# Optimization experiments

Hardware: AMD Instinct MI355X
Metric: run time of the kernel (lower is better)

The kernel has to match this reference:

```python
import jax, jax.numpy as jnp
import numpy as np

N = 100000   # nodes
E = 1600000  # edges (avg degree 16)
IN, HID, OUT = 128, 128, 64


def _glorot(key, shape):
    limit = np.sqrt(6.0 / (shape[0] + shape[1])).astype(np.float32)
    return jax.random.uniform(key, shape, jnp.float32, -limit, limit)


def setup_inputs() -> dict:
    key = jax.random.key(0)
    ks = jax.random.split(key, 12)
    inp = {}
    for i, (f, s, d) in enumerate([("feat1", "src1", "dst1"), ("feat2", "src2", "dst2"), ("feat", "src", "dst")]):
        inp[f] = jax.random.normal(ks[3 * i], (N, IN), jnp.float32)
        inp[s] = jax.random.randint(ks[3 * i + 1], (E,), 0, N, jnp.int32)
        inp[d] = jax.random.randint(ks[3 * i + 2], (E,), 0, N, jnp.int32)
    inp["W1"] = _glorot(ks[9], (IN, HID))
    inp["b1"] = jnp.zeros((HID,), jnp.float32)
    inp["W2"] = _glorot(ks[10], (HID, OUT))
    inp["b2"] = jnp.zeros((OUT,), jnp.float32)
    return inp


def _gcn_layer(x, src, dst, W, b):
    # DGL GraphConv norm='both': D_dst^{-1/2} * A * D_src^{-1/2} * X * W + b
    ones = jnp.ones(src.shape, jnp.float32)
    deg_out = jax.ops.segment_sum(ones, src, num_segments=N)
    deg_in = jax.ops.segment_sum(ones, dst, num_segments=N)
    norm_src = jax.lax.rsqrt(jnp.maximum(deg_out, 1.0))
    norm_dst = jax.lax.rsqrt(jnp.maximum(deg_in, 1.0))
    h = (x @ W) * norm_src[:, None]           # transform then normalize (math-equivalent order)
    agg = jax.ops.segment_sum(h[src], dst, num_segments=N)  # spmm aggregate
    return agg * norm_dst[:, None] + b


def _encoder(x, src, dst, W1, b1, W2, b2):
    h = jax.nn.relu(_gcn_layer(x, src, dst, W1, b1))
    return _gcn_layer(h, src, dst, W2, b2)


def reference(feat1, src1, dst1, feat2, src2, dst2, feat, src, dst, W1, b1, W2, b2):
    z1 = _encoder(feat1, src1, dst1, W1, b1, W2, b2)
    z2 = _encoder(feat2, src2, dst2, W1, b1, W2, b2)
    z = _encoder(feat, src, dst, W1, b1, W2, b2)
    return (z1, z2, z)
```

## Files before the change

### kernel.cpp

```cpp
#include <hip/hip_runtime.h>

#define NNODES 100000
#define NEDGES 1600000
#define FIN 128
#define FHID 128
#define FOUT 64

typedef unsigned short u16;
typedef unsigned char u8;
typedef unsigned int u32;
typedef __attribute__((ext_vector_type(8))) short short8;
typedef __attribute__((ext_vector_type(4))) float floatx4;

#define NBUK 391
#define NSL2 250
#define SLICE2 (NEDGES / NSL2)
#define SP ((size_t)NSL2 * NBUK)
#define NH16 ((size_t)NNODES * FHID)

__device__ __forceinline__ u16 f2bf(float f) {
  u32 u = __float_as_uint(f);
  u32 r = (u + 0x7fffu + ((u >> 16) & 1u)) >> 16;
  return (u16)r;
}

__device__ __forceinline__ const int* sel(const int* a, const int* b, const int* c, int z) {
  return z == 0 ? a : (z == 1 ? b : c);
}


__global__ __launch_bounds__(256) void bucket_hist_kernel(
    const int* s0, const int* s1, const int* s2,
    const int* d0, const int* d1, const int* d2,
    u16* __restrict__ Hbase, int E) {
  const int z = blockIdx.z;
  const int* __restrict__ src = sel(s0, s1, s2, z);
  const int* __restrict__ dst = sel(d0, d1, d2, z);
  u32* __restrict__ part = (u32*)(Hbase + (size_t)z * NH16);
  u32* __restrict__ part_src = part + SP;
  __shared__ u32 hd[NBUK], hs[NBUK];
  const int s = blockIdx.x;
  for (int i = threadIdx.x; i < NBUK; i += 256) { hd[i] = 0; hs[i] = 0; }
  __syncthreads();
  const int e0 = s * SLICE2, e1 = min(e0 + SLICE2, E);
  const int i0 = e0 >> 2, i1 = e1 >> 2;
  for (int i = i0 + threadIdx.x; i < i1; i += 256) {
    int4 dv = ((const int4*)dst)[i];
    int4 sv = ((const int4*)src)[i];
    atomicAdd(&hd[(u32)dv.x >> 8], 1u);
    atomicAdd(&hd[(u32)dv.y >> 8], 1u);
    atomicAdd(&hd[(u32)dv.z >> 8], 1u);
    atomicAdd(&hd[(u32)dv.w >> 8], 1u);
    atomicAdd(&hs[(u32)sv.x >> 8], 1u);
    atomicAdd(&hs[(u32)sv.y >> 8], 1u);
    atomicAdd(&hs[(u32)sv.z >> 8], 1u);
    atomicAdd(&hs[(u32)sv.w >> 8], 1u);
  }
  __syncthreads();
  for (int i = threadIdx.x; i < NBUK; i += 256) {
    part[(size_t)s * NBUK + i] = hd[i];
    part_src[(size_t)s * NBUK + i] = hs[i];
  }
}

__global__ __launch_bounds__(512) void scan_part_kernel(u16* __restrict__ Hbase,
                                                        u32* __restrict__ boff_d,
                                                        u32* __restrict__ bcount_d,
                                                        u32* __restrict__ boff_s,
                                                        u32* __restrict__ bcount_s) {
  const int z = blockIdx.z;
  u32* base = (u32*)(Hbase + (size_t)z * NH16);
  u32* __restrict__ part = blockIdx.x ? base + SP : base;
  u32* __restrict__ boff = (blockIdx.x ? boff_s : boff_d) + (size_t)z * NBUK;
  u32* __restrict__ bcount = (blockIdx.x ? bcount_s : bcount_d) + (size_t)z * NBUK;
  const int b = threadIdx.x;
  u32 run = 0;
  if (b < NBUK) {
#pragma unroll 5
    for (int s = 0; s < NSL2; s++) {
      u32 v = part[(size_t)s * NBUK + b];
      part[(size_t)s * NBUK + b] = run;
      run += v;
    }
  }
  __shared__ u32 sh[512];
  sh[threadIdx.x] = (b < NBUK) ? run : 0;
  __syncthreads();
  for (int d = 1; d < 512; d <<= 1) {
    u32 t = (threadIdx.x >= d) ? sh[threadIdx.x - d] : 0;
    __syncthreads();
    sh[threadIdx.x] += t;
    __syncthreads();
  }
  if (b < NBUK) {
    boff[b] = sh[threadIdx.x] - run;
    bcount[b] = run;
  }
}

__global__ __launch_bounds__(256) void scatter_kernel(
    const int* s0, const int* s1, const int* s2,
    const int* d0, const int* d1, const int* d2,
    u16* __restrict__ Hbase, u16* __restrict__ Tbase,
    const u32* __restrict__ boff_d, const u32* __restrict__ boff_src, int E) {
  const int z = blockIdx.z;
  const int* __restrict__ src = sel(s0, s1, s2, z);
  const int* __restrict__ dst = sel(d0, d1, d2, z);
  const u32* __restrict__ part = (const u32*)(Hbase + (size_t)z * NH16);
  const u32* __restrict__ part_src = part + SP;
  u8* __restrict__ pes = (u8*)(part_src + SP);
  u32* __restrict__ pe = (u32*)(Tbase + (size_t)z * NH16);
  const u32* __restrict__ boff = boff_d + (size_t)z * NBUK;
  const u32* __restrict__ boff_s = boff_src + (size_t)z * NBUK;
  __shared__ u32 cur[NBUK], curs[NBUK];
  const int s = blockIdx.x;
  for (int i = threadIdx.x; i < NBUK; i += 256) {
    cur[i] = part[(size_t)s * NBUK + i] + boff[i];
    curs[i] = part_src[(size_t)s * NBUK + i] + boff_s[i];
  }
  __syncthreads();
  const int e0 = s * SLICE2, e1 = min(e0 + SLICE2, E);
  const int i0 = e0 >> 2, i1 = e1 >> 2;
  for (int i = i0 + threadIdx.x; i < i1; i += 256) {
    int4 sv = ((const int4*)src)[i];
    int4 dv = ((const int4*)dst)[i];
    u32 p;
    p = atomicAdd(&cur[(u32)dv.x >> 8], 1u); pe[p] = ((u32)sv.x << 8) | ((u32)dv.x & 255u);
    p = atomicAdd(&cur[(u32)dv.y >> 8], 1u); pe[p] = ((u32)sv.y << 8) | ((u32)dv.y & 255u);
    p = atomicAdd(&cur[(u32)dv.z >> 8], 1u); pe[p] = ((u32)sv.z << 8) | ((u32)dv.z & 255u);
    p = atomicAdd(&cur[(u32)dv.w >> 8], 1u); pe[p] = ((u32)sv.w << 8) | ((u32)dv.w & 255u);
    p = atomicAdd(&curs[(u32)sv.x >> 8], 1u); pes[p] = (u8)((u32)sv.x & 255u);
    p = atomicAdd(&curs[(u32)sv.y >> 8], 1u); pes[p] = (u8)((u32)sv.y & 255u);
    p = atomicAdd(&curs[(u32)sv.z >> 8], 1u); pes[p] = (u8)((u32)sv.z & 255u);
    p = atomicAdd(&curs[(u32)sv.w >> 8], 1u); pes[p] = (u8)((u32)sv.w & 255u);
  }
}

__global__ __launch_bounds__(256) void bucket_csr_kernel(const u16* __restrict__ Tbase,
                                                         const u32* __restrict__ boffb,
                                                         const u32* __restrict__ bcountb,
                                                         int* __restrict__ csrb,
                                                         int* __restrict__ offsb,
                                                         int* __restrict__ degb,
                                                         float* __restrict__ ndb, int n) {
  const int z = blockIdx.z;
  const u32* __restrict__ pe = (const u32*)(Tbase + (size_t)z * NH16);
  int* __restrict__ csr = csrb + (size_t)z * NEDGES;
  int* __restrict__ offs = offsb + (size_t)z * NNODES;
  int* __restrict__ deg_dst = degb + (size_t)z * NNODES;
  float* __restrict__ norm_dst = ndb + (size_t)z * NNODES;
  const u32* boff = boffb + (size_t)z * NBUK;
  const u32* bcount = bcountb + (size_t)z * NBUK;
  const int b = blockIdx.x;
  const int beg = (int)boff[b];
  const int cnt = (int)bcount[b];
  __shared__ int h[256], loc[256];
  const int t = threadIdx.x;
  h[t] = 0;
  __syncthreads();
  for (int i = t; i < cnt; i += 256) atomicAdd(&h[pe[beg + i] & 255u], 1);
  __syncthreads();
  const int myc = h[t];
  loc[t] = myc;
  __syncthreads();
  for (int d = 1; d < 256; d <<= 1) {
    int v = (t >= d) ? loc[t - d] : 0;
    __syncthreads();
    loc[t] += v;
    __syncthreads();
  }
  const int start = beg + loc[t] - myc;
  const int node = b * 256 + t;
  if (node < n) {
    offs[node] = start;
    deg_dst[node] = myc;
    norm_dst[node] = rsqrtf(fmaxf((float)myc, 1.0f));
  }
  __syncthreads();
  h[t] = start;
  __syncthreads();
  for (int i = t; i < cnt; i += 256) {
    u32 v = pe[beg + i];
    int p = atomicAdd(&h[v & 255u], 1);
    csr[p] = (int)(v >> 8);
  }
}

__global__ __launch_bounds__(256) void bucket_count_src_kernel(const u16* __restrict__ Hbase,
                                                               const u32* __restrict__ boffb,
                                                               const u32* __restrict__ bcountb,
                                                               float* __restrict__ nsb, int n) {
  const int z = blockIdx.z;
  const u32* partb = (const u32*)(Hbase + (size_t)z * NH16);
  const u8* __restrict__ pes = (const u8*)(partb + 2 * SP);
  const u32* boff = boffb + (size_t)z * NBUK;
  const u32* bcount = bcountb + (size_t)z * NBUK;
  float* __restrict__ norm_src = nsb + (size_t)z * NNODES;
  const int b = blockIdx.x;
  const int beg = (int)boff[b];
  const int cnt = (int)bcount[b];
  __shared__ int h[256];
  h[threadIdx.x] = 0;
  __syncthreads();
  for (int i = threadIdx.x; i < cnt; i += 256) atomicAdd(&h[pes[beg + i]], 1);
  __syncthreads();
  const int node = b * 256 + threadIdx.x;
  if (node < n) norm_src[node] = rsqrtf(fmaxf((float)h[threadIdx.x], 1.0f));
}


#define XP 136

template <int CTOT, bool IN_BF16>
__global__ __launch_bounds__(256) void gemm_mfma(const void* X0, const void* X1,
                                                 const void* X2,
                                                 const float* __restrict__ W,
                                                 const float* __restrict__ normb,
                                                 u16* __restrict__ Yb, int nrows) {
  const int z = blockIdx.z;
  const void* __restrict__ Xv = z == 0 ? X0 : (z == 1 ? X1 : X2);
  const float* __restrict__ norm = normb + (size_t)z * NNODES;
  u16* __restrict__ Y = Yb + (size_t)z * NNODES * CTOT;
  __shared__ u16 Xs[64 * XP];
  __shared__ u16 Wt[64 * XP];
  __shared__ float norm_s[64];
  const int tid = threadIdx.x;
  const int row0 = blockIdx.x * 64;
  const int col0 = blockIdx.y * 64;

  if constexpr (IN_BF16) {
    const u16* X = (const u16*)Xv;
    for (int i = tid; i < 64 * 16; i += 256) {
      int r = i >> 4, k8 = (i & 15) * 8;
      int gr = row0 + r;
      uint4 v = make_uint4(0u, 0u, 0u, 0u);
      if (gr < nrows) v = *(const uint4*)&X[(size_t)gr * 128 + k8];
      *(uint4*)&Xs[r * XP + k8] = v;
    }
  } else {
    const float* X = (const float*)Xv;
    for (int i = tid; i < 64 * 32; i += 256) {
      int r = i >> 5, k4 = (i & 31) * 4;
      int gr = row0 + r;
      ushort4 o = make_ushort4(0, 0, 0, 0);
      if (gr < nrows) {
        float4 v = *(const float4*)&X[(size_t)gr * 128 + k4];
        o.x = f2bf(v.x); o.y = f2bf(v.y); o.z = f2bf(v.z); o.w = f2bf(v.w);
      }
      *(ushort4*)&Xs[r * XP + k4] = o;
    }
  }
  for (int i = tid; i < 128 * 16; i += 256) {
    int k = i >> 4, c4 = (i & 15) * 4;
    float4 v = *(const float4*)&W[(size_t)k * CTOT + col0 + c4];
    Wt[(c4 + 0) * XP + k] = f2bf(v.x);
    Wt[(c4 + 1) * XP + k] = f2bf(v.y);
    Wt[(c4 + 2) * XP + k] = f2bf(v.z);
    Wt[(c4 + 3) * XP + k] = f2bf(v.w);
  }
  if (tid < 64) norm_s[tid] = (row0 + tid < nrows) ? norm[row0 + tid] : 0.f;
  __syncthreads();

  const int w = tid >> 6, lane = tid & 63;
  const int quad = lane >> 4, r16 = lane & 15;
  const int arow = w * 16 + r16;

  short8 a[4];
#pragma unroll
  for (int kc = 0; kc < 4; kc++)
    a[kc] = *(const short8*)&Xs[arow * XP + kc * 32 + quad * 8];

#pragma unroll
  for (int nc = 0; nc < 4; nc++) {
    floatx4 acc = {0.f, 0.f, 0.f, 0.f};
#pragma unroll
    for (int kc = 0; kc < 4; kc++) {
      short8 b = *(const short8*)&Wt[(nc * 16 + r16) * XP + kc * 32 + quad * 8];
      acc = __builtin_amdgcn_mfma_f32_16x16x32_bf16(a[kc], b, acc, 0, 0, 0);
    }
#pragma unroll
    for (int i = 0; i < 4; i++) {
      int lr = w * 16 + quad * 4 + i;
      int gr = row0 + lr;
      if (gr < nrows)
        Y[(size_t)gr * CTOT + col0 + nc * 16 + r16] = f2bf(acc[i] * norm_s[lr]);
    }
  }
}


__device__ __forceinline__ void acc_row(float* acc, uint4 p) {
  acc[0] += __uint_as_float(p.x << 16);
  acc[1] += __uint_as_float(p.x & 0xffff0000u);
  acc[2] += __uint_as_float(p.y << 16);
  acc[3] += __uint_as_float(p.y & 0xffff0000u);
  acc[4] += __uint_as_float(p.z << 16);
  acc[5] += __uint_as_float(p.z & 0xffff0000u);
  acc[6] += __uint_as_float(p.w << 16);
  acc[7] += __uint_as_float(p.w & 0xffff0000u);
}

template <int F, bool RELU, bool OUT_BF16>
__global__ __launch_bounds__(256) void spmm_bf16(const u16* __restrict__ Hbase,
                                                 const int* __restrict__ offsb,
                                                 const int* __restrict__ degb,
                                                 const int* __restrict__ csrb,
                                                 const float* __restrict__ ndb,
                                                 const float* __restrict__ bias,
                                                 void* __restrict__ Yv, int n) {
  const int z = blockIdx.z;
  const u16* __restrict__ Hb = Hbase + (size_t)z * NNODES * F;
  const int* __restrict__ offs = offsb + (size_t)z * NNODES;
  const int* __restrict__ deg = degb + (size_t)z * NNODES;
  const int* __restrict__ csr = csrb + (size_t)z * NEDGES;
  const float* __restrict__ norm_dst = ndb + (size_t)z * NNODES;
  constexpr int TPN = F / 8;
  constexpr int NPB = 256 / TPN;
  int node = blockIdx.x * NPB + threadIdx.x / TPN;
  if (node >= n) return;
  int f0 = (threadIdx.x % TPN) * 8;
  int beg = offs[node];
  int end = beg + deg[node];
  const u16* __restrict__ Hp = Hb + f0;
  float acc[8] = {};
  int e = beg;
  int nfull = (end - beg) >> 2;
  if (nfull > 0) {
    int sv[4]; uint4 p[4];
#pragma unroll
    for (int j = 0; j < 4; j++) sv[j] = csr[e + j];
#pragma unroll
    for (int j = 0; j < 4; j++) p[j] = *(const uint4*)&Hp[(size_t)sv[j] * F];
    for (int b = 1; b < nfull; b++) {
      e += 4;
      int s2[4]; uint4 q[4];
#pragma unroll
      for (int j = 0; j < 4; j++) s2[j] = csr[e + j];
#pragma unroll
      for (int j = 0; j < 4; j++) q[j] = *(const uint4*)&Hp[(size_t)s2[j] * F];
#pragma unroll
      for (int j = 0; j < 4; j++) acc_row(acc, p[j]);
#pragma unroll
      for (int j = 0; j < 4; j++) p[j] = q[j];
    }
#pragma unroll
    for (int j = 0; j < 4; j++) acc_row(acc, p[j]);
    e += 4;
  }
  for (; e < end; e++) {
    int s = csr[e];
    uint4 p = *(const uint4*)&Hp[(size_t)s * F];
    acc_row(acc, p);
  }
  float nd = norm_dst[node];
  float o[8];
#pragma unroll
  for (int i = 0; i < 8; i++) {
    o[i] = fmaf(acc[i], nd, bias[f0 + i]);
    if (RELU) o[i] = fmaxf(o[i], 0.f);
  }
  if constexpr (OUT_BF16) {
    u16* Y = (u16*)Yv + (size_t)z * NNODES * F;
    uint4 pk;
    pk.x = (u32)f2bf(o[0]) | ((u32)f2bf(o[1]) << 16);
    pk.y = (u32)f2bf(o[2]) | ((u32)f2bf(o[3]) << 16);
    pk.z = (u32)f2bf(o[4]) | ((u32)f2bf(o[5]) << 16);
    pk.w = (u32)f2bf(o[6]) | ((u32)f2bf(o[7]) << 16);
    *(uint4*)&Y[(size_t)node * F + f0] = pk;
  } else {
    float* Y = (float*)Yv + (size_t)z * NNODES * F;
    *(float4*)&Y[(size_t)node * F + f0] = make_float4(o[0], o[1], o[2], o[3]);
    *(float4*)&Y[(size_t)node * F + f0 + 4] = make_float4(o[4], o[5], o[6], o[7]);
  }
}


extern "C" void kernel_launch(void* const* d_in, const int* in_sizes, int n_in,
                              void* d_out, int out_size, void* d_ws, size_t ws_size,
                              hipStream_t stream) {
  const int N = NNODES;
  const int E = NEDGES;
  const float* W1 = (const float*)d_in[9];
  const float* b1 = (const float*)d_in[10];
  const float* W2 = (const float*)d_in[11];
  const float* b2 = (const float*)d_in[12];

  const size_t HBYTES = NH16 * 2;

  auto need_for = [&](size_t NG) -> size_t {
    size_t o = 0;
    auto al = [&](size_t b) { o = (o + b + 255) & ~(size_t)255; };
    al(NG * N * 4);
    al(NG * N * 4);
    al(NG * N * 4);
    al(NG * N * 4);
    al(NG * NBUK * 4);
    al(NG * NBUK * 4);
    al(NG * NBUK * 4);
    al(NG * NBUK * 4);
    al(NG * (size_t)E * 4);
    al(NG * HBYTES);
    al(NG * HBYTES);
    return o;
  };
  const bool batched = ws_size >= need_for(3);
  const size_t NG = batched ? 3 : 1;

  char* ws = (char*)d_ws;
  size_t off = 0;
  auto alloc = [&](size_t bytes) -> void* {
    void* p = ws + off;
    off += (bytes + 255) & ~(size_t)255;
    return p;
  };
  int* deg_dst = (int*)alloc(NG * N * 4);
  float* norm_src = (float*)alloc(NG * N * 4);
  float* norm_dst = (float*)alloc(NG * N * 4);
  int* offs = (int*)alloc(NG * N * 4);
  u32* boff = (u32*)alloc(NG * NBUK * 4);
  u32* bcount = (u32*)alloc(NG * NBUK * 4);
  u32* boff_s = (u32*)alloc(NG * NBUK * 4);
  u32* bcount_s = (u32*)alloc(NG * NBUK * 4);
  int* csr = (int*)alloc(NG * (size_t)E * 4);
  u16* H = (u16*)alloc(NG * HBYTES);
  u16* T = (u16*)alloc(NG * HBYTES);

  const int gemm_rb = (N + 63) / 64;
  const int nb1 = (N + 15) / 16;
  const int nb2 = (N + 31) / 32;

  auto run = [&](const int* s0, const int* s1, const int* s2,
                 const int* d0, const int* d1, const int* d2,
                 const float* f0, const float* f1, const float* f2,
                 const void* x20, const void* x21, const void* x22,
                 void* zoutv, unsigned gz) {
    bucket_hist_kernel<<<dim3(NSL2, 1, gz), 256, 0, stream>>>(s0, s1, s2, d0, d1, d2, H, E);
    scan_part_kernel<<<dim3(2, 1, gz), 512, 0, stream>>>(H, boff, bcount, boff_s, bcount_s);
    scatter_kernel<<<dim3(NSL2, 1, gz), 256, 0, stream>>>(s0, s1, s2, d0, d1, d2,
                                                          H, T, boff, boff_s, E);
    bucket_csr_kernel<<<dim3(NBUK, 1, gz), 256, 0, stream>>>(T, boff, bcount, csr, offs,
                                                             deg_dst, norm_dst, N);
    bucket_count_src_kernel<<<dim3(NBUK, 1, gz), 256, 0, stream>>>(H, boff_s, bcount_s,
                                                                   norm_src, N);
    gemm_mfma<FHID, false><<<dim3(gemm_rb, FHID / 64, gz), 256, 0, stream>>>(
        f0, f1, f2, W1, norm_src, H, N);
    spmm_bf16<FHID, true, true><<<dim3(nb1, 1, gz), 256, 0, stream>>>(
        H, offs, deg_dst, csr, norm_dst, b1, T, N);
    gemm_mfma<FOUT, true><<<dim3(gemm_rb, FOUT / 64, gz), 256, 0, stream>>>(
        x20, x21, x22, W2, norm_src, H, N);
    spmm_bf16<FOUT, false, false><<<dim3(nb2, 1, gz), 256, 0, stream>>>(
        H, offs, deg_dst, csr, norm_dst, b2, zoutv, N);
  };

  if (batched) {
    run((const int*)d_in[1], (const int*)d_in[4], (const int*)d_in[7],
        (const int*)d_in[2], (const int*)d_in[5], (const int*)d_in[8],
        (const float*)d_in[0], (const float*)d_in[3], (const float*)d_in[6],
        T, T + NH16, T + 2 * NH16,
        d_out, 3);
  } else {
    for (int g = 0; g < 3; g++) {
      const float* feat = (const float*)d_in[3 * g + 0];
      const int* src = (const int*)d_in[3 * g + 1];
      const int* dst = (const int*)d_in[3 * g + 2];
      float* zout = (float*)d_out + (size_t)g * N * FOUT;
      run(src, src, src, dst, dst, dst, feat, feat, feat, T, T, T, zout, 1);
    }
  }
}
```

Before: 713.3 us.

## Sort nodes by in-degree within buckets for balanced SpMM and merge finish kernels

```diff
diff --git a/kernel.cpp b/kernel.cpp
--- a/kernel.cpp
+++ b/kernel.cpp
@@ -13,6 +13,7 @@
 typedef __attribute__((ext_vector_type(4))) float floatx4;
 
 #define NBUK 391
+#define NPAD2 (NBUK * 256)
 #define NSL2 250
 #define SLICE2 (NEDGES / NSL2)
 #define SP ((size_t)NSL2 * NBUK)
@@ -136,26 +137,43 @@
   }
 }
 
-__global__ __launch_bounds__(256) void bucket_csr_kernel(const u16* __restrict__ Tbase,
-                                                         const u32* __restrict__ boffb,
-                                                         const u32* __restrict__ bcountb,
-                                                         int* __restrict__ csrb,
-                                                         int* __restrict__ offsb,
-                                                         int* __restrict__ degb,
-                                                         float* __restrict__ ndb, int n) {
-  const int z = blockIdx.z;
+__global__ __launch_bounds__(256) void bucket_finish_kernel(
+    const u16* __restrict__ Tbase, const u16* __restrict__ Hbase,
+    const u32* __restrict__ boffb, const u32* __restrict__ bcountb,
+    const u32* __restrict__ boff_sb, const u32* __restrict__ bcount_sb,
+    int* __restrict__ csrb, int* __restrict__ offsb, int* __restrict__ degb,
+    float* __restrict__ ndb, float* __restrict__ nsb, int* __restrict__ permb, int n) {
+  const int z = blockIdx.z;
+  const int b = blockIdx.x;
+  const int t = threadIdx.x;
+  if (blockIdx.y == 1) {
+    const u32* partb = (const u32*)(Hbase + (size_t)z * NH16);
+    const u8* __restrict__ pes = (const u8*)(partb + 2 * SP);
+    const u32* boff = boff_sb + (size_t)z * NBUK;
+    const u32* bcount = bcount_sb + (size_t)z * NBUK;
+    float* __restrict__ norm_src = nsb + (size_t)z * NNODES;
+    const int beg = (int)boff[b];
+    const int cnt = (int)bcount[b];
+    __shared__ int hh[256];
+    hh[t] = 0;
+    __syncthreads();
+    for (int i = t; i < cnt; i += 256) atomicAdd(&hh[pes[beg + i]], 1);
+    __syncthreads();
+    const int node = b * 256 + t;
+    if (node < n) norm_src[node] = rsqrtf(fmaxf((float)hh[t], 1.0f));
+    return;
+  }
   const u32* __restrict__ pe = (const u32*)(Tbase + (size_t)z * NH16);
   int* __restrict__ csr = csrb + (size_t)z * NEDGES;
   int* __restrict__ offs = offsb + (size_t)z * NNODES;
   int* __restrict__ deg_dst = degb + (size_t)z * NNODES;
   float* __restrict__ norm_dst = ndb + (size_t)z * NNODES;
+  int* __restrict__ perm = permb + (size_t)z * NPAD2;
   const u32* boff = boffb + (size_t)z * NBUK;
   const u32* bcount = bcountb + (size_t)z * NBUK;
-  const int b = blockIdx.x;
   const int beg = (int)boff[b];
   const int cnt = (int)bcount[b];
   __shared__ int h[256], loc[256];
-  const int t = threadIdx.x;
   h[t] = 0;
   __syncthreads();
   for (int i = t; i < cnt; i += 256) atomicAdd(&h[pe[beg + i] & 255u], 1);
@@ -176,6 +194,22 @@
     deg_dst[node] = myc;
     norm_dst[node] = rsqrtf(fmaxf((float)myc, 1.0f));
   }
+  __shared__ int dh[64], dbase[64], cnt2[64];
+  const int dg = myc > 63 ? 63 : myc;
+  if (t < 64) { dh[t] = 0; cnt2[t] = 0; }
+  __syncthreads();
+  atomicAdd(&dh[dg], 1);
+  __syncthreads();
+  if (t < 64) dbase[t] = dh[t];
+  __syncthreads();
+  for (int d = 1; d < 64; d <<= 1) {
+    int v = (t >= d && t < 64) ? dbase[t - d] : 0;
+    __syncthreads();
+    if (t < 64) dbase[t] += v;
+    __syncthreads();
+  }
+  const int rank = dbase[dg] - dh[dg] + atomicAdd(&cnt2[dg], 1);
+  perm[b * 256 + rank] = node;
   __syncthreads();
   h[t] = start;
   __syncthreads();
@@ -184,28 +218,6 @@
     int p = atomicAdd(&h[v & 255u], 1);
     csr[p] = (int)(v >> 8);
   }
-}
-
-__global__ __launch_bounds__(256) void bucket_count_src_kernel(const u16* __restrict__ Hbase,
-                                                               const u32* __restrict__ boffb,
-                                                               const u32* __restrict__ bcountb,
-                                                               float* __restrict__ nsb, int n) {
-  const int z = blockIdx.z;
-  const u32* partb = (const u32*)(Hbase + (size_t)z * NH16);
-  const u8* __restrict__ pes = (const u8*)(partb + 2 * SP);
-  const u32* boff = boffb + (size_t)z * NBUK;
-  const u32* bcount = bcountb + (size_t)z * NBUK;
-  float* __restrict__ norm_src = nsb + (size_t)z * NNODES;
-  const int b = blockIdx.x;
-  const int beg = (int)boff[b];
-  const int cnt = (int)bcount[b];
-  __shared__ int h[256];
-  h[threadIdx.x] = 0;
-  __syncthreads();
-  for (int i = threadIdx.x; i < cnt; i += 256) atomicAdd(&h[pes[beg + i]], 1);
-  __syncthreads();
-  const int node = b * 256 + threadIdx.x;
-  if (node < n) norm_src[node] = rsqrtf(fmaxf((float)h[threadIdx.x], 1.0f));
 }
 
 
@@ -307,6 +319,7 @@
                                                  const int* __restrict__ csrb,
                                                  const float* __restrict__ ndb,
                                                  const float* __restrict__ bias,
+                                                 const int* __restrict__ permb,
                                                  void* __restrict__ Yv, int n) {
   const int z = blockIdx.z;
   const u16* __restrict__ Hb = Hbase + (size_t)z * NNODES * F;
@@ -314,9 +327,12 @@
   const int* __restrict__ deg = degb + (size_t)z * NNODES;
   const int* __restrict__ csr = csrb + (size_t)z * NEDGES;
   const float* __restrict__ norm_dst = ndb + (size_t)z * NNODES;
+  const int* __restrict__ perm = permb + (size_t)z * NPAD2;
   constexpr int TPN = F / 8;
   constexpr int NPB = 256 / TPN;
-  int node = blockIdx.x * NPB + threadIdx.x / TPN;
+  int idx = blockIdx.x * NPB + threadIdx.x / TPN;
+  if (idx >= NPAD2) return;
+  int node = perm[idx];
   if (node >= n) return;
   int f0 = (threadIdx.x % TPN) * 8;
   int beg = offs[node];
@@ -398,6 +414,7 @@
     al(NG * NBUK * 4);
     al(NG * NBUK * 4);
     al(NG * NBUK * 4);
+    al(NG * (size_t)NPAD2 * 4);
     al(NG * (size_t)E * 4);
     al(NG * HBYTES);
     al(NG * HBYTES);
@@ -421,13 +438,14 @@
   u32* bcount = (u32*)alloc(NG * NBUK * 4);
   u32* boff_s = (u32*)alloc(NG * NBUK * 4);
   u32* bcount_s = (u32*)alloc(NG * NBUK * 4);
+  int* perm = (int*)alloc(NG * (size_t)NPAD2 * 4);
   int* csr = (int*)alloc(NG * (size_t)E * 4);
   u16* H = (u16*)alloc(NG * HBYTES);
   u16* T = (u16*)alloc(NG * HBYTES);
 
   const int gemm_rb = (N + 63) / 64;
-  const int nb1 = (N + 15) / 16;
-  const int nb2 = (N + 31) / 32;
+  const int nb1 = NPAD2 / 16;
+  const int nb2 = NPAD2 / 32;
 
   auto run = [&](const int* s0, const int* s1, const int* s2,
                  const int* d0, const int* d1, const int* d2,
@@ -438,18 +456,17 @@
     scan_part_kernel<<<dim3(2, 1, gz), 512, 0, stream>>>(H, boff, bcount, boff_s, bcount_s);
     scatter_kernel<<<dim3(NSL2, 1, gz), 256, 0, stream>>>(s0, s1, s2, d0, d1, d2,
                                                           H, T, boff, boff_s, E);
-    bucket_csr_kernel<<<dim3(NBUK, 1, gz), 256, 0, stream>>>(T, boff, bcount, csr, offs,
-                                                             deg_dst, norm_dst, N);
-    bucket_count_src_kernel<<<dim3(NBUK, 1, gz), 256, 0, stream>>>(H, boff_s, bcount_s,
-                                                                   norm_src, N);
+    bucket_finish_kernel<<<dim3(NBUK, 2, gz), 256, 0, stream>>>(
+        T, H, boff, bcount, boff_s, bcount_s, csr, offs, deg_dst, norm_dst,
+        norm_src, perm, N);
     gemm_mfma<FHID, false><<<dim3(gemm_rb, FHID / 64, gz), 256, 0, stream>>>(
         f0, f1, f2, W1, norm_src, H, N);
     spmm_bf16<FHID, true, true><<<dim3(nb1, 1, gz), 256, 0, stream>>>(
-        H, offs, deg_dst, csr, norm_dst, b1, T, N);
+        H, offs, deg_dst, csr, norm_dst, b1, perm, T, N);
     gemm_mfma<FOUT, true><<<dim3(gemm_rb, FOUT / 64, gz), 256, 0, stream>>>(
         x20, x21, x22, W2, norm_src, H, N);
     spmm_bf16<FOUT, false, false><<<dim3(nb2, 1, gz), 256, 0, stream>>>(
-        H, offs, deg_dst, csr, norm_dst, b2, zoutv, N);
+        H, offs, deg_dst, csr, norm_dst, b2, perm, d_out ? zoutv : zoutv, N);
   };
 
   if (batched) {
```

New measurement: 768.0 us. 7.7% more time.
